# Optimization experiments

Hardware: AMD Instinct MI355X
Metric: run time of the kernel (lower is better)

## Reference

```python
import jax, jax.numpy as jnp
import numpy as np

N_USERS = 100000
N_ITEMS = 50000
N_NODES = N_USERS + N_ITEMS
D = 32
N_EDGES = 8000000
N_LAYERS = 3
B = 65536


def setup_inputs() -> dict:
    key = jax.random.key(0)
    ks = jax.random.split(key, 9)
    users = jax.random.randint(ks[0], (B,), 0, N_USERS)
    items = jax.random.randint(ks[1], (B,), 0, N_ITEMS)
    # COO sparse normalized adjacency (symmetric bipartite graph in LightGCN)
    rows = jax.random.randint(ks[2], (N_EDGES,), 0, N_NODES)
    cols = jax.random.randint(ks[3], (N_EDGES,), 0, N_NODES)
    # normalized values ~ 1/sqrt(deg_i*deg_j); keep small so propagation is stable
    vals = jax.random.uniform(ks[4], (N_EDGES,), dtype=jnp.float32) * 0.01
    # embedding tables, init std=0.1 per nn.init.normal_(std=0.1)
    user_emb = jax.random.normal(ks[5], (N_USERS, D), dtype=jnp.float32) * 0.1
    item_emb = jax.random.normal(ks[6], (N_ITEMS, D), dtype=jnp.float32) * 0.1
    # per-user denormalization stats (norm_mode='users')
    norm_means = jax.random.normal(ks[7], (N_USERS,), dtype=jnp.float32)
    norm_stds = jax.random.uniform(ks[8], (N_USERS,), dtype=jnp.float32) + 0.5
    return {
        "users": users, "items": items,
        "rows": rows, "cols": cols, "vals": vals,
        "user_emb": user_emb, "item_emb": item_emb,
        "norm_means": norm_means, "norm_stds": norm_stds,
    }


def _spmm(rows, cols, vals, x):
    # sparse COO matmul: out[i] = sum_{e: rows[e]==i} vals[e] * x[cols[e]]
    return jax.ops.segment_sum(vals[:, None] * x[cols], rows, num_segments=N_NODES)


def reference(users, items, rows, cols, vals, user_emb, item_emb, norm_means, norm_stds):
    all_emb = jnp.concatenate([user_emb, item_emb], axis=0)  # [N, D]
    acc = all_emb
    emb_sum = all_emb
    for _ in range(N_LAYERS):
        acc = _spmm(rows, cols, vals, acc)
        emb_sum = emb_sum + acc
    light_out = emb_sum / jnp.asarray(N_LAYERS + 1, dtype=all_emb.dtype)
    all_users = light_out[:N_USERS]
    all_items = light_out[N_USERS:]
    gamma = jnp.sum(all_users[users] * all_items[items], axis=1)  # [B]
    # norm_mode == 'users' -> index stats by users
    return gamma * norm_stds[users] + norm_means[users]
```

## Files before the change

kernel.cpp:

```cpp
#include <hip/hip_runtime.h>
#include <hip/hip_fp16.h>

#define N_USERS 100000
#define N_ITEMS 50000
#define N_NODES 150000
#define DIM 32
#define N_EDGES 8000000
#define B_OUT 65536

#define NB 1024
#define RPB 147
#define CH 16384
#define N_PBLK ((N_EDGES + CH - 1) / CH)
#define PART_T 1024
#define EPT (CH / PART_T)
#define MS_T 512
#define T 256
#define NRED 8
#define RS_LD (NB + 1)
#define NPANEL 3
#define NBIN (RPB * NPANEL)
#define BUFE 8448
#define VQ_SCALE 1638400.0f
#define VQ_INV   6.103515625e-7f
#define WSCALE1 (VQ_INV * 8.0f)
#define WSCALE2 (VQ_INV * 32.0f)
#define WSCALE3 (VQ_INV * 32.0f)
#define INV1 (1.0f / 64.0f)
#define INV2 (1.0f / 2048.0f)
#define INV3 (1.0f / 65536.0f)

__device__ __forceinline__ unsigned enc_h(unsigned u16) {
    return (u16 + 0x7Fu + ((u16 >> 8) & 1u)) >> 8;
}
__device__ __forceinline__ unsigned enc_f(float x) {
    return enc_h((unsigned)__half_as_ushort(__float2half(x)));
}
__device__ __forceinline__ float dec_b(unsigned b) {
    return __half2float(__ushort_as_half((unsigned short)(b << 8)));
}
__device__ __forceinline__ int panel_of(int col) {
    return (col >= 100000) ? 2 : ((col >= 50000) ? 1 : 0);
}

__global__ void init_kernel(const float* __restrict__ user_emb,
                            const float* __restrict__ item_emb,
                            unsigned char* __restrict__ x_a) {
    int i = blockIdx.x * blockDim.x + threadIdx.x;
    const int total = N_NODES * DIM / 8;
    if (i >= total) return;
    const int user8 = N_USERS * DIM / 8;
    const float4* src = (i < user8) ? ((const float4*)user_emb + (size_t)i * 2)
                                    : ((const float4*)item_emb + (size_t)(i - user8) * 2);
    float4 a = src[0], b = src[1];
    unsigned w0 = enc_f(a.x * 8.f) | (enc_f(a.y * 8.f) << 8)
                | (enc_f(a.z * 8.f) << 16) | (enc_f(a.w * 8.f) << 24);
    unsigned w1 = enc_f(b.x * 8.f) | (enc_f(b.y * 8.f) << 8)
                | (enc_f(b.z * 8.f) << 16) | (enc_f(b.w * 8.f) << 24);
    uint2 o; o.x = w0; o.y = w1;
    ((uint2*)x_a)[i] = o;
}

__global__ void __launch_bounds__(PART_T)
part_kernel(const int* __restrict__ rows,
            const int* __restrict__ cols,
            const float* __restrict__ vals,
            int* __restrict__ runstart,
            int2* __restrict__ bucket_ev) {
    __shared__ int2 buf[CH];
    __shared__ int hist[NB];
    __shared__ int wsum[16];
    const int tid   = threadIdx.x;
    const int chunk = blockIdx.x;
    const int e0    = chunk * CH;
    const int ecnt  = (N_EDGES - e0 < CH) ? (N_EDGES - e0) : CH;
    const int lane  = tid & 63, wid = tid >> 6;

    hist[tid] = 0;
    __syncthreads();

    int myrow[EPT];
    #pragma unroll
    for (int j = 0; j < EPT; ++j) {
        int idx = j * PART_T + tid;
        int r = (idx < ecnt) ? rows[e0 + idx] : -1;
        myrow[j] = r;
        if (r >= 0) atomicAdd(&hist[(unsigned)r / RPB], 1);
    }
    __syncthreads();

    int v = hist[tid];
    int inc = v;
    #pragma unroll
    for (int off = 1; off < 64; off <<= 1) {
        int t = __shfl_up(inc, off, 64);
        if (lane >= off) inc += t;
    }
    if (lane == 63) wsum[wid] = inc;
    __syncthreads();
    if (wid == 0) {
        int s = (lane < 16) ? wsum[lane] : 0;
        #pragma unroll
        for (int off = 1; off < 16; off <<= 1) {
            int t = __shfl_up(s, off, 64);
            if (lane >= off) s += t;
        }
        if (lane < 16) wsum[lane] = s;
    }
    __syncthreads();
    int base = (wid > 0) ? wsum[wid - 1] : 0;
    int incl = base + inc;
    int excl = incl - v;
    runstart[(size_t)chunk * RS_LD + tid] = e0 + excl;
    if (tid == NB - 1) runstart[(size_t)chunk * RS_LD + NB] = e0 + incl;
    hist[tid] = excl;
    __syncthreads();

    #pragma unroll
    for (int j = 0; j < EPT; ++j) {
        int r = myrow[j];
        if (r < 0) continue;
        int idx = j * PART_T + tid;
        unsigned b = (unsigned)r / RPB;
        int k = atomicAdd(&hist[b], 1);
        int2 ev;
        ev.x = (int)(((unsigned)(r - (int)b * RPB) << 18) | (unsigned)cols[e0 + idx]);
        ev.y = __float_as_int(vals[e0 + idx]);
        buf[k] = ev;
    }
    __syncthreads();

    const int n4 = ecnt >> 1;
    const int4* b4 = (const int4*)buf;
    int4* g4 = (int4*)(bucket_ev + e0);
    for (int i = tid; i < n4; i += PART_T) g4[i] = b4[i];
}

__global__ void btot_kernel(const int* __restrict__ runstart, int* __restrict__ partial) {
    const int b = threadIdx.x;
    const int g = blockIdx.x;
    int c = 0;
    for (int ch = g; ch < N_PBLK; ch += NRED)
        c += runstart[(size_t)ch * RS_LD + b + 1] - runstart[(size_t)ch * RS_LD + b];
    partial[g * NB + b] = c;
}

__global__ void bscan_kernel(const int* __restrict__ partial,
                             int* __restrict__ bcsr,
                             int* __restrict__ row_ptr) {
    __shared__ int wsum[16];
    const int tid = threadIdx.x;
    const int lane = tid & 63, wid = tid >> 6;
    int v = 0;
    #pragma unroll
    for (int g = 0; g < NRED; ++g) v += partial[g * NB + tid];
    int inc = v;
    #pragma unroll
    for (int off = 1; off < 64; off <<= 1) {
        int t = __shfl_up(inc, off, 64);
        if (lane >= off) inc += t;
    }
    if (lane == 63) wsum[wid] = inc;
    __syncthreads();
    if (wid == 0) {
        int s = (lane < 16) ? wsum[lane] : 0;
        #pragma unroll
        for (int off = 1; off < 16; off <<= 1) {
            int t = __shfl_up(s, off, 64);
            if (lane >= off) s += t;
        }
        if (lane < 16) wsum[lane] = s;
    }
    __syncthreads();
    int base = (wid > 0) ? wsum[wid - 1] : 0;
    bcsr[tid] = base + inc - v;
    if (tid == 0) row_ptr[N_NODES] = N_EDGES;
}

__global__ void __launch_bounds__(MS_T)
mini_scatter_kernel(const int* __restrict__ runstart,
                    const int2* __restrict__ bucket_ev,
                    const int* __restrict__ bcsr,
                    int* __restrict__ row_ptr,
                    unsigned* __restrict__ csr_w) {
    __shared__ unsigned sbuf[BUFE];
    __shared__ int rs0[N_PBLK];
    __shared__ int rs1[N_PBLK];
    __shared__ int cnt2[NBIN];
    __shared__ int cur2[NBIN];
    __shared__ int wsum[MS_T / 64];
    __shared__ int stot;
    const int b   = blockIdx.x;
    const int tid = threadIdx.x;
    const int lane = tid & 63, wid = tid >> 6;

    for (int i = tid; i < N_PBLK; i += MS_T) {
        rs0[i] = runstart[(size_t)i * RS_LD + b];
        rs1[i] = runstart[(size_t)i * RS_LD + b + 1];
    }
    if (tid < NBIN) cnt2[tid] = 0;
    __syncthreads();

    const int grp = tid >> 4, ln = tid & 15;
    for (int c = grp; c < N_PBLK; c += (MS_T / 16))
        for (int i = rs0[c] + ln; i < rs1[c]; i += 16) {
            unsigned key = (unsigned)bucket_ev[i].x;
            int rl  = (int)(key >> 18);
            int col = (int)(key & 0x3FFFFu);
            atomicAdd(&cnt2[rl * NPANEL + panel_of(col)], 1);
        }
    __syncthreads();

    int v = (tid < NBIN) ? cnt2[tid] : 0;
    int inc = v;
    #pragma unroll
    for (int off = 1; off < 64; off <<= 1) {
        int t = __shfl_up(inc, off, 64);
        if (lane >= off) inc += t;
    }
    if (lane == 63) wsum[wid] = inc;
    __syncthreads();
    if (wid == 0) {
        int s = (lane < MS_T / 64) ? wsum[lane] : 0;
        #pragma unroll
        for (int off = 1; off < MS_T / 64; off <<= 1) {
            int t = __shfl_up(s, off, 64);
            if (lane >= off) s += t;
        }
        if (lane < MS_T / 64) wsum[lane] = s;
    }
    __syncthreads();
    const int cb = bcsr[b];
    int base = (wid > 0) ? wsum[wid - 1] : 0;
    if (tid == NBIN - 1) stot = base + inc;
    if (tid < NBIN) {
        int excl = base + inc - v;
        cur2[tid] = excl;
        if (tid % NPANEL == 0) {
            int r = b * RPB + tid / NPANEL;
            if (r < N_NODES) row_ptr[r] = cb + excl;
        }
    }
    __syncthreads();
    const int cnt = stot;

    if (cnt <= BUFE) {
        for (int c = grp; c < N_PBLK; c += (MS_T / 16))
            for (int i = rs0[c] + ln; i < rs1[c]; i += 16) {
                int2 ev = bucket_ev[i];
                unsigned key = (unsigned)ev.x;
                int rl  = (int)(key >> 18);
                int col = (int)(key & 0x3FFFFu);
                float vv = __int_as_float(ev.y);
                int q = (int)(vv * VQ_SCALE + 0.5f);
                if (q > 16383) q = 16383;
                int pos = atomicAdd(&cur2[rl * NPANEL + panel_of(col)], 1);
                sbuf[pos] = ((unsigned)col << 14) | (unsigned)q;
            }
        __syncthreads();
        unsigned* g = csr_w + cb;
        for (int i = tid; i < cnt; i += MS_T) g[i] = sbuf[i];
    } else {
        for (int c = grp; c < N_PBLK; c += (MS_T / 16))
            for (int i = rs0[c] + ln; i < rs1[c]; i += 16) {
                int2 ev = bucket_ev[i];
                unsigned key = (unsigned)ev.x;
                int rl  = (int)(key >> 18);
                int col = (int)(key & 0x3FFFFu);
                float vv = __int_as_float(ev.y);
                int q = (int)(vv * VQ_SCALE + 0.5f);
                if (q > 16383) q = 16383;
                int pos = atomicAdd(&cur2[rl * NPANEL + panel_of(col)], 1);
                csr_w[cb + pos] = ((unsigned)col << 14) | (unsigned)q;
            }
    }
}

__global__ void spmm_kernel(const int* __restrict__ row_ptr,
                            const unsigned* __restrict__ csr,
                            const unsigned char* __restrict__ xin,
                            unsigned char* __restrict__ xout,
                            float wscale) {
    int tid = blockIdx.x * blockDim.x + threadIdx.x;
    int row = tid >> 5;
    if (row >= N_NODES) return;
    const int ll  = tid & 31;
    const int j   = ll >> 2;
    const int seg = ll & 3;
    const int s = row_ptr[row];
    const int e = row_ptr[row + 1];

    __half2 acc0 = __float2half2_rn(0.f);
    __half2 acc1 = acc0, acc2 = acc0, acc3 = acc0;

    for (int i = s; i < e; i += 16) {
        int ea = i + j;
        int eb = i + 8 + j;
        unsigned pa = (ea < e) ? csr[ea] : 0u;
        unsigned pb = (eb < e) ? csr[eb] : 0u;
        const uint2* qa = (const uint2*)(xin + (size_t)(pa >> 14) * 32) + seg;
        const uint2* qb = (const uint2*)(xin + (size_t)(pb >> 14) * 32) + seg;
        uint2 va = *qa;
        uint2 vb = *qb;
        __half2 wa = __float2half2_rn((float)(pa & 0x3FFFu) * wscale);
        __half2 wb = __float2half2_rn((float)(pb & 0x3FFFu) * wscale);
        unsigned h;
        h = ((va.x & 0xFFu) << 8) | ((va.x & 0xFF00u) << 16);
        acc0 = __hfma2(wa, *(__half2*)&h, acc0);
        h = ((va.x >> 8) & 0xFF00u) | (va.x & 0xFF000000u);
        acc1 = __hfma2(wa, *(__half2*)&h, acc1);
        h = ((va.y & 0xFFu) << 8) | ((va.y & 0xFF00u) << 16);
        acc2 = __hfma2(wa, *(__half2*)&h, acc2);
        h = ((va.y >> 8) & 0xFF00u) | (va.y & 0xFF000000u);
        acc3 = __hfma2(wa, *(__half2*)&h, acc3);
        h = ((vb.x & 0xFFu) << 8) | ((vb.x & 0xFF00u) << 16);
        acc0 = __hfma2(wb, *(__half2*)&h, acc0);
        h = ((vb.x >> 8) & 0xFF00u) | (vb.x & 0xFF000000u);
        acc1 = __hfma2(wb, *(__half2*)&h, acc1);
        h = ((vb.y & 0xFFu) << 8) | ((vb.y & 0xFF00u) << 16);
        acc2 = __hfma2(wb, *(__half2*)&h, acc2);
        h = ((vb.y >> 8) & 0xFF00u) | (vb.y & 0xFF000000u);
        acc3 = __hfma2(wb, *(__half2*)&h, acc3);
    }

    #pragma unroll
    for (int m = 4; m <= 16; m <<= 1) {
        unsigned t;
        t = (unsigned)__shfl_xor(*(int*)&acc0, m, 64); acc0 = __hadd2(acc0, *(__half2*)&t);
        t = (unsigned)__shfl_xor(*(int*)&acc1, m, 64); acc1 = __hadd2(acc1, *(__half2*)&t);
        t = (unsigned)__shfl_xor(*(int*)&acc2, m, 64); acc2 = __hadd2(acc2, *(__half2*)&t);
        t = (unsigned)__shfl_xor(*(int*)&acc3, m, 64); acc3 = __hadd2(acc3, *(__half2*)&t);
    }

    if (j == 0) {
        unsigned a0 = *(unsigned*)&acc0, a1 = *(unsigned*)&acc1;
        unsigned a2 = *(unsigned*)&acc2, a3 = *(unsigned*)&acc3;
        unsigned w0 = enc_h(a0 & 0xFFFFu) | (enc_h(a0 >> 16) << 8)
                    | (enc_h(a1 & 0xFFFFu) << 16) | (enc_h(a1 >> 16) << 24);
        unsigned w1 = enc_h(a2 & 0xFFFFu) | (enc_h(a2 >> 16) << 8)
                    | (enc_h(a3 & 0xFFFFu) << 16) | (enc_h(a3 >> 16) << 24);
        uint2 o; o.x = w0; o.y = w1;
        *(uint2*)(xout + (size_t)row * 32 + seg * 8) = o;
    }
}

__device__ __forceinline__ void add_row8(float* s, const unsigned char* x,
                                         size_t node, float inv) {
    const uint4* p = (const uint4*)(x + node * 32);
    uint4 t0 = p[0], t1 = p[1];
    unsigned w[8] = {t0.x, t0.y, t0.z, t0.w, t1.x, t1.y, t1.z, t1.w};
    #pragma unroll
    for (int k = 0; k < 8; ++k) {
        unsigned ww = w[k];
        s[k * 4 + 0] += dec_b(ww & 0xFFu) * inv;
        s[k * 4 + 1] += dec_b((ww >> 8) & 0xFFu) * inv;
        s[k * 4 + 2] += dec_b((ww >> 16) & 0xFFu) * inv;
        s[k * 4 + 3] += dec_b(ww >> 24) * inv;
    }
}

__global__ void final_kernel(const int* __restrict__ users,
                             const int* __restrict__ items,
                             const float* __restrict__ user_emb,
                             const float* __restrict__ item_emb,
                             const unsigned char* __restrict__ x1,
                             const unsigned char* __restrict__ x2,
                             const unsigned char* __restrict__ x3,
                             const float* __restrict__ means,
                             const float* __restrict__ stds,
                             float* __restrict__ out) {
    int b = blockIdx.x * blockDim.x + threadIdx.x;
    if (b >= B_OUT) return;
    int u  = users[b];
    int itm = items[b];
    size_t un = (size_t)u;
    size_t in = (size_t)(N_USERS + itm);

    float su[DIM], si[DIM];
    const float4* eu = (const float4*)(user_emb + un * DIM);
    const float4* ei = (const float4*)(item_emb + (size_t)itm * DIM);
    #pragma unroll
    for (int k = 0; k < 8; ++k) {
        float4 a = eu[k];
        su[k * 4 + 0] = a.x; su[k * 4 + 1] = a.y; su[k * 4 + 2] = a.z; su[k * 4 + 3] = a.w;
        float4 c = ei[k];
        si[k * 4 + 0] = c.x; si[k * 4 + 1] = c.y; si[k * 4 + 2] = c.z; si[k * 4 + 3] = c.w;
    }
    add_row8(su, x1, un, INV1); add_row8(su, x2, un, INV2); add_row8(su, x3, un, INV3);
    add_row8(si, x1, in, INV1); add_row8(si, x2, in, INV2); add_row8(si, x3, in, INV3);

    float gamma = 0.f;
    #pragma unroll
    for (int d = 0; d < DIM; ++d) gamma += su[d] * si[d];
    gamma *= 0.0625f;
    out[b] = gamma * stds[u] + means[u];
}

extern "C" void kernel_launch(void* const* d_in, const int* in_sizes, int n_in,
                              void* d_out, int out_size, void* d_ws, size_t ws_size,
                              hipStream_t stream) {
    const int*   users    = (const int*)d_in[0];
    const int*   items    = (const int*)d_in[1];
    const int*   rows     = (const int*)d_in[2];
    const int*   cols     = (const int*)d_in[3];
    const float* vals     = (const float*)d_in[4];
    const float* user_emb = (const float*)d_in[5];
    const float* item_emb = (const float*)d_in[6];
    const float* means    = (const float*)d_in[7];
    const float* stds     = (const float*)d_in[8];
    float* out = (float*)d_out;

    char* w = (char*)d_ws;
    size_t off = 0;
    auto alloc = [&](size_t bytes) -> void* {
        void* p = w + off;
        off = (off + bytes + 255) & ~(size_t)255;
        return p;
    };
    size_t regionA = ((size_t)N_PBLK * CH * sizeof(int2) + 255) & ~(size_t)255;
    char* a0 = (char*)alloc(regionA);
    int2* bucket_ev = (int2*)a0;
    size_t aoff = 0;
    auto allocA = [&](size_t bytes) -> void* {
        void* p = a0 + aoff;
        aoff = (aoff + bytes + 255) & ~(size_t)255;
        return p;
    };
    unsigned char* x_a = (unsigned char*)allocA((size_t)N_NODES * DIM);
    unsigned char* x_b = (unsigned char*)allocA((size_t)N_NODES * DIM);
    unsigned char* x_c = (unsigned char*)allocA((size_t)N_NODES * DIM);
    unsigned char* x_d = (unsigned char*)allocA((size_t)N_NODES * DIM);

    int*      runstart = (int*)     alloc((size_t)N_PBLK * RS_LD * sizeof(int));
    int*      partial  = (int*)     alloc((size_t)NRED * NB * sizeof(int));
    int*      row_ptr  = (int*)     alloc((size_t)(N_NODES + 1) * sizeof(int));
    int*      bcsr     = (int*)     alloc((size_t)NB * sizeof(int));
    unsigned* csr_w    = (unsigned*)alloc((size_t)N_EDGES * sizeof(unsigned));
    (void)ws_size;

    const int g_init  = (N_NODES * DIM / 8 + T - 1) / T;
    const int g_spmm  = (N_NODES * DIM + T - 1) / T;
    const int g_final = (B_OUT + T - 1) / T;

    part_kernel<<<N_PBLK, PART_T, 0, stream>>>(rows, cols, vals, runstart, bucket_ev);
    btot_kernel<<<NRED, NB, 0, stream>>>(runstart, partial);
    bscan_kernel<<<1, NB, 0, stream>>>(partial, bcsr, row_ptr);
    mini_scatter_kernel<<<NB, MS_T, 0, stream>>>(runstart, bucket_ev, bcsr, row_ptr, csr_w);

    init_kernel<<<g_init, T, 0, stream>>>(user_emb, item_emb, x_a);
    spmm_kernel<<<g_spmm, T, 0, stream>>>(row_ptr, csr_w, x_a, x_b, WSCALE1);
    spmm_kernel<<<g_spmm, T, 0, stream>>>(row_ptr, csr_w, x_b, x_c, WSCALE2);
    spmm_kernel<<<g_spmm, T, 0, stream>>>(row_ptr, csr_w, x_c, x_d, WSCALE3);

    final_kernel<<<g_final, T, 0, stream>>>(users, items, user_emb, item_emb,
                                            x_b, x_c, x_d, means, stds, out);
}
```

Measured before the change: 305.6 us.

## Stage bucket runs in LDS once and halve partition chunk size

The mini-scatter kernel first prefix-sums the per-chunk run lengths, then copies all of its bucket entries from global memory into a shared-memory buffer once. The counting and scatter passes now read that buffer instead of reading global memory twice. The partition chunk size is halved and the scatter block size doubled, which changes how many runs each block handles and how many threads serve them. The 64 KB staging buffer raises LDS use per block and may reduce occupancy, and smaller chunks double the runstart table size.

```diff
diff --git a/kernel.cpp b/kernel.cpp
--- a/kernel.cpp
+++ b/kernel.cpp
@@ -10,11 +10,11 @@
 
 #define NB 1024
 #define RPB 147
-#define CH 16384
+#define CH 8192
 #define N_PBLK ((N_EDGES + CH - 1) / CH)
 #define PART_T 1024
 #define EPT (CH / PART_T)
-#define MS_T 512
+#define MS_T 1024
 #define T 256
 #define NRED 8
 #define RS_LD (NB + 1)
@@ -183,42 +183,34 @@
                     const int* __restrict__ bcsr,
                     int* __restrict__ row_ptr,
                     unsigned* __restrict__ csr_w) {
+    __shared__ int2 ibuf[BUFE];
     __shared__ unsigned sbuf[BUFE];
     __shared__ int rs0[N_PBLK];
-    __shared__ int rs1[N_PBLK];
+    __shared__ int ofs[N_PBLK];
+    __shared__ int rlen[N_PBLK];
     __shared__ int cnt2[NBIN];
     __shared__ int cur2[NBIN];
     __shared__ int wsum[MS_T / 64];
-    __shared__ int stot;
     const int b   = blockIdx.x;
     const int tid = threadIdx.x;
     const int lane = tid & 63, wid = tid >> 6;
 
     for (int i = tid; i < N_PBLK; i += MS_T) {
-        rs0[i] = runstart[(size_t)i * RS_LD + b];
-        rs1[i] = runstart[(size_t)i * RS_LD + b + 1];
+        int a = runstart[(size_t)i * RS_LD + b];
+        rs0[i]  = a;
+        rlen[i] = runstart[(size_t)i * RS_LD + b + 1] - a;
     }
     if (tid < NBIN) cnt2[tid] = 0;
     __syncthreads();
 
-    const int grp = tid >> 4, ln = tid & 15;
-    for (int c = grp; c < N_PBLK; c += (MS_T / 16))
-        for (int i = rs0[c] + ln; i < rs1[c]; i += 16) {
-            unsigned key = (unsigned)bucket_ev[i].x;
-            int rl  = (int)(key >> 18);
-            int col = (int)(key & 0x3FFFFu);
-            atomicAdd(&cnt2[rl * NPANEL + panel_of(col)], 1);
-        }
-    __syncthreads();
-
-    int v = (tid < NBIN) ? cnt2[tid] : 0;
-    int inc = v;
+    int lv = (tid < N_PBLK) ? rlen[tid] : 0;
+    int linc = lv;
     #pragma unroll
     for (int off = 1; off < 64; off <<= 1) {
-        int t = __shfl_up(inc, off, 64);
-        if (lane >= off) inc += t;
-    }
-    if (lane == 63) wsum[wid] = inc;
+        int t = __shfl_up(linc, off, 64);
+        if (lane >= off) linc += t;
+    }
+    if (lane == 63) wsum[wid] = linc;
     __syncthreads();
     if (wid == 0) {
         int s = (lane < MS_T / 64) ? wsum[lane] : 0;
@@ -230,9 +222,56 @@
         if (lane < MS_T / 64) wsum[lane] = s;
     }
     __syncthreads();
+    int lbase = (wid > 0) ? wsum[wid - 1] : 0;
+    if (tid < N_PBLK) ofs[tid] = lbase + linc - lv;
+    __syncthreads();
+    const int cnt = ofs[N_PBLK - 1] + rlen[N_PBLK - 1];
+    __syncthreads();
+
+    const int grp8 = tid >> 3, ln8 = tid & 7;
     const int cb = bcsr[b];
+
+    if (cnt <= BUFE) {
+        for (int c = grp8; c < N_PBLK; c += (MS_T / 8)) {
+            int s0 = rs0[c], o0 = ofs[c], L = rlen[c];
+            for (int i = ln8; i < L; i += 8) ibuf[o0 + i] = bucket_ev[s0 + i];
+        }
+        __syncthreads();
+        for (int i = tid; i < cnt; i += MS_T) {
+            unsigned key = (unsigned)ibuf[i].x;
+            atomicAdd(&cnt2[((int)(key >> 18)) * NPANEL + panel_of((int)(key & 0x3FFFFu))], 1);
+        }
+    } else {
+        for (int c = grp8; c < N_PBLK; c += (MS_T / 8)) {
+            int s0 = rs0[c], L = rlen[c];
+            for (int i = ln8; i < L; i += 8) {
+                unsigned key = (unsigned)bucket_ev[s0 + i].x;
+                atomicAdd(&cnt2[((int)(key >> 18)) * NPANEL + panel_of((int)(key & 0x3FFFFu))], 1);
+            }
+        }
+    }
+    __syncthreads();
+
+    int v = (tid < NBIN) ? cnt2[tid] : 0;
+    int inc = v;
+    #pragma unroll
+    for (int off = 1; off < 64; off <<= 1) {
+        int t = __shfl_up(inc, off, 64);
+        if (lane >= off) inc += t;
+    }
+    if (lane == 63) wsum[wid] = inc;
+    __syncthreads();
+    if (wid == 0) {
+        int s = (lane < MS_T / 64) ? wsum[lane] : 0;
+        #pragma unroll
+        for (int off = 1; off < MS_T / 64; off <<= 1) {
+            int t = __shfl_up(s, off, 64);
+            if (lane >= off) s += t;
+        }
+        if (lane < MS_T / 64) wsum[lane] = s;
+    }
+    __syncthreads();
     int base = (wid > 0) ? wsum[wid - 1] : 0;
-    if (tid == NBIN - 1) stot = base + inc;
     if (tid < NBIN) {
         int excl = base + inc - v;
         cur2[tid] = excl;
@@ -242,28 +281,27 @@
         }
     }
     __syncthreads();
-    const int cnt = stot;
 
     if (cnt <= BUFE) {
-        for (int c = grp; c < N_PBLK; c += (MS_T / 16))
-            for (int i = rs0[c] + ln; i < rs1[c]; i += 16) {
-                int2 ev = bucket_ev[i];
-                unsigned key = (unsigned)ev.x;
-                int rl  = (int)(key >> 18);
-                int col = (int)(key & 0x3FFFFu);
-                float vv = __int_as_float(ev.y);
-                int q = (int)(vv * VQ_SCALE + 0.5f);
-                if (q > 16383) q = 16383;
-                int pos = atomicAdd(&cur2[rl * NPANEL + panel_of(col)], 1);
-                sbuf[pos] = ((unsigned)col << 14) | (unsigned)q;
-            }
+        for (int i = tid; i < cnt; i += MS_T) {
+            int2 ev = ibuf[i];
+            unsigned key = (unsigned)ev.x;
+            int rl  = (int)(key >> 18);
+            int col = (int)(key & 0x3FFFFu);
+            float vv = __int_as_float(ev.y);
+            int q = (int)(vv * VQ_SCALE + 0.5f);
+            if (q > 16383) q = 16383;
+            int pos = atomicAdd(&cur2[rl * NPANEL + panel_of(col)], 1);
+            sbuf[pos] = ((unsigned)col << 14) | (unsigned)q;
+        }
         __syncthreads();
         unsigned* g = csr_w + cb;
         for (int i = tid; i < cnt; i += MS_T) g[i] = sbuf[i];
     } else {
-        for (int c = grp; c < N_PBLK; c += (MS_T / 16))
-            for (int i = rs0[c] + ln; i < rs1[c]; i += 16) {
-                int2 ev = bucket_ev[i];
+        for (int c = grp8; c < N_PBLK; c += (MS_T / 8)) {
+            int s0 = rs0[c], L = rlen[c];
+            for (int i = ln8; i < L; i += 8) {
+                int2 ev = bucket_ev[s0 + i];
                 unsigned key = (unsigned)ev.x;
                 int rl  = (int)(key >> 18);
                 int col = (int)(key & 0x3FFFFu);
@@ -273,6 +311,7 @@
                 int pos = atomicAdd(&cur2[rl * NPANEL + panel_of(col)], 1);
                 csr_w[cb + pos] = ((unsigned)col << 14) | (unsigned)q;
             }
+        }
     }
 }
 
```

Measured after the change: 301.5 us. About the same (-1.3%).
